# Performance work log

Measured on AMD Instinct MI355X. Metric: run time of the kernel, lower is better.

The kernel has to match this reference:

```python
import jax, jax.numpy as jnp
import numpy as np


def setup_inputs() -> dict:
    key = jax.random.key(0)
    k1, k2, k3 = jax.random.split(key, 3)
    N = 16384
    y = jax.random.normal(k1, (N,), dtype=jnp.float32)
    y_hat = jax.random.normal(k2, (N,), dtype=jnp.float32)
    status = jax.random.randint(k3, (N,), 0, 2, dtype=jnp.int32)
    return {"y": y, "y_hat": y_hat, "status": status}


def reference(y, y_hat, status):
    # Pairwise concordance index over all pairs i < j.
    # ge[i, j] = y[i] >= y[j]; le[i, j] = y[i] <= y[j]
    N = y.shape[0]
    ge = y[:, None] >= y[None, :]
    le = y[:, None] <= y[None, :]
    ge_hat = y_hat[:, None] >= y_hat[None, :]
    le_hat = y_hat[:, None] <= y_hat[None, :]
    st_i = (status == 1)[:, None]  # astatus_1 broadcast over j
    st_j = (status == 1)[None, :]  # bstatus_1 broadcast over i
    # upper-triangular mask (strict): pairs with j > i
    mask = jnp.triu(jnp.ones((N, N), dtype=bool), k=1)

    c1 = ge & ge_hat & st_j
    c2 = le & le_hat & st_i
    cc = (c1 | c2) & mask

    tp1 = le & st_i
    tp2 = ge & st_j
    tp = (tp1 | tp2) & mask

    c = jnp.sum(cc.astype(jnp.int32)).astype(jnp.float32)
    total_pairs = jnp.sum(tp.astype(jnp.int32)).astype(jnp.float32)
    return c / total_pairs
```

## Files before the change

kernel.cpp:

```cpp
#include <hip/hip_runtime.h>


#define BLOCK 256
#define TI 256
#define TJ 512
#define GRID_MAIN 1024


__global__ __launch_bounds__(256) void compact_kernel(
    const float* __restrict__ y, const float* __restrict__ yh,
    const int* __restrict__ status, int n,
    unsigned* __restrict__ cnts,
    float* __restrict__ y1, float* __restrict__ yh1,
    float* __restrict__ y0, float* __restrict__ yh0)
{
    int i = blockIdx.x * 256 + threadIdx.x;
    int lane = threadIdx.x & 63;
    bool act = i < n;
    float yv  = act ? y[i]  : 0.0f;
    float yhv = act ? yh[i] : 0.0f;
    bool st = act && (status[i] == 1);
    unsigned long long m1 = __ballot(st);
    unsigned long long m0 = __ballot(act && !st);
    unsigned long long lt = (lane == 63) ? ~0ull >> 1 : ((1ull << lane) - 1ull);
    unsigned b1 = 0, b0 = 0;
    if (lane == 0) {
        b1 = atomicAdd(&cnts[0], (unsigned)__popcll(m1));
        b0 = atomicAdd(&cnts[1], (unsigned)__popcll(m0));
    }
    b1 = __shfl(b1, 0, 64);
    b0 = __shfl(b0, 0, 64);
    if (st) {
        unsigned s = b1 + (unsigned)__popcll(m1 & lt);
        y1[s] = yv; yh1[s] = yhv;
    } else if (act) {
        unsigned s = b0 + (unsigned)__popcll(m0 & lt);
        y0[s] = yv; yh0[s] = yhv;
    }
}

__global__ __launch_bounds__(BLOCK) void pairs_kernel(
    const unsigned* __restrict__ cnts,
    const float* __restrict__ y1, const float* __restrict__ yh1,
    const float* __restrict__ y0, const float* __restrict__ yh0,
    unsigned long long* __restrict__ acc)
{
    __shared__ __align__(16) float2 s_yy[TJ];
    const int tid = threadIdx.x;
    const unsigned K = cnts[0], M = cnts[1];
    const int ntJ  = (int)((K + TJ - 1) / TJ);
    const int ntIA = (int)((K + TI - 1) / TI);
    const int ntIB = (int)((M + TI - 1) / TI);
    const int ntA  = ntIA * ntJ;
    const int ntot = ntA + ntIB * ntJ;

    const float PINF = __int_as_float(0x7f800000);
    const float NINF = __int_as_float(0xff800000);

    unsigned accA = 0, accBc = 0, accBt = 0;

    for (int t = blockIdx.x; t < ntot; t += gridDim.x) {
        bool isA = t < ntA;
        int tt = isA ? t : t - ntA;
        int ti = tt / ntJ;
        int tj = tt - ti * ntJ;
        int jbase = tj * TJ;
        int jcnt = (int)K - jbase; if (jcnt > TJ) jcnt = TJ;

        for (int s = tid; s < TJ; s += BLOCK) {
            bool inb = s < jcnt;
            int j = jbase + s;
            float a = inb ? y1[j]  : PINF;
            float b = inb ? yh1[j] : NINF;
            s_yy[s] = make_float2(a, b);
        }
        __syncthreads();

        int i = ti * TI + tid;
        unsigned ilim = isA ? K : M;
        const float* py = isA ? y1  : y0;
        const float* ph = isA ? yh1 : yh0;
        bool iv = (unsigned)i < ilim;
        float yi  = iv ? py[i] : NINF;
        float yhi = iv ? ph[i] : NINF;

        if (isA) {
            unsigned ax = 0;
#pragma unroll 8
            for (int jj = 0; jj < TJ; ++jj) {
                float2 p = s_yy[jj];
                ax += (unsigned)((yi >= p.x) != (yhi >= p.y));
            }
            if (iv) accA += (unsigned)TJ - ax;
        } else {
            unsigned bg = 0, bc = 0;
#pragma unroll 8
            for (int jj = 0; jj < TJ; ++jj) {
                float2 p = s_yy[jj];
                bool ge = yi >= p.x;
                bool gh = yhi >= p.y;
                bg += (unsigned)ge;
                bc += (unsigned)(ge & gh);
            }
            accBt += bg; accBc += bc;
        }
        __syncthreads();
    }

#pragma unroll
    for (int off = 32; off > 0; off >>= 1) {
        accA  += __shfl_down(accA,  off, 64);
        accBc += __shfl_down(accBc, off, 64);
        accBt += __shfl_down(accBt, off, 64);
    }
    __shared__ unsigned rA[4], rC[4], rT[4];
    int wav = tid >> 6, lane = tid & 63;
    if (lane == 0) { rA[wav] = accA; rC[wav] = accBc; rT[wav] = accBt; }
    __syncthreads();
    if (tid == 0) {
        unsigned long long a = rA[0] + rA[1] + rA[2] + rA[3];
        unsigned long long c = rC[0] + rC[1] + rC[2] + rC[3];
        unsigned long long t = rT[0] + rT[1] + rT[2] + rT[3];
        if (a) atomicAdd(&acc[0], a);
        if (c) atomicAdd(&acc[1], c);
        if (t) atomicAdd(&acc[2], t);
    }
}

__global__ void finalize_kernel(const unsigned* __restrict__ cnts,
                                const unsigned long long* __restrict__ acc,
                                float* __restrict__ out)
{
    if (threadIdx.x == 0) {
        unsigned long long K = cnts[0];
        unsigned long long CC = acc[0] + 2ull * acc[1];
        unsigned long long TP = K * K + 2ull * acc[2];
        long long cn = (long long)CC - (long long)K;
        long long tn = (long long)TP - (long long)K;
        out[0] = (float)cn / (float)tn;
    }
}

extern "C" void kernel_launch(void* const* d_in, const int* in_sizes, int n_in,
                              void* d_out, int out_size, void* d_ws, size_t ws_size,
                              hipStream_t stream) {
    const float* y      = (const float*)d_in[0];
    const float* y_hat  = (const float*)d_in[1];
    const int*   status = (const int*)d_in[2];
    float* out = (float*)d_out;
    int n = in_sizes[0];

    char* base = (char*)d_ws;
    unsigned* cnts = (unsigned*)base;
    unsigned long long* acc = (unsigned long long*)(base + 8);
    float* y1  = (float*)(base + 64);
    float* yh1 = y1 + n;
    float* y0  = yh1 + n;
    float* yh0 = y0 + n;

    hipMemsetAsync(base, 0, 32, stream);

    hipLaunchKernelGGL(compact_kernel, dim3((n + 255) / 256), dim3(256), 0, stream,
                       y, y_hat, status, n, cnts, y1, yh1, y0, yh0);

    hipLaunchKernelGGL(pairs_kernel, dim3(GRID_MAIN), dim3(BLOCK), 0, stream,
                       cnts, y1, yh1, y0, yh0, acc);

    hipLaunchKernelGGL(finalize_kernel, dim3(1), dim3(64), 0, stream,
                       cnts, acc, out);
}
```

Measured before the change: 94.94 us.

## Register-block four i-values per thread and pad compacted arrays with sentinels

Each thread now holds four i elements in registers, so every shared-memory j load is reused four times and the LDS read traffic per comparison falls. The y and y_hat arrays are interleaved into float2 and padded to multiples of 1024 with infinity sentinels written by a new fill kernel. This removes the bounds checks in the tile loads, and the padding contribution is subtracted analytically in finalize. The cost is a larger i-tile, which can waste work on padding and lowers the number of tiles, plus an extra kernel that fills the workspace.

```diff
diff --git a/kernel.cpp b/kernel.cpp
--- a/kernel.cpp
+++ b/kernel.cpp
@@ -2,17 +2,29 @@
 
 
 #define BLOCK 256
-#define TI 256
-#define TJ 512
-#define GRID_MAIN 1024
+#define TJ 256
+#define IT 4
+#define TI (BLOCK * IT)
+#define GRID_PAIRS 1024
 
+
+__global__ __launch_bounds__(256) void fill_kernel(
+    float2* __restrict__ p1, float2* __restrict__ p0, int stride,
+    unsigned* __restrict__ hdr)
+{
+    int i = blockIdx.x * 256 + threadIdx.x;
+    if (i < stride) {
+        p1[i] = make_float2(__int_as_float(0x7f800000), __int_as_float(0xff800000));
+        p0[i] = make_float2(__int_as_float(0xff800000), __int_as_float(0xff800000));
+    }
+    if (blockIdx.x == 0 && threadIdx.x < 8) hdr[threadIdx.x] = 0u;
+}
 
 __global__ __launch_bounds__(256) void compact_kernel(
     const float* __restrict__ y, const float* __restrict__ yh,
     const int* __restrict__ status, int n,
     unsigned* __restrict__ cnts,
-    float* __restrict__ y1, float* __restrict__ yh1,
-    float* __restrict__ y0, float* __restrict__ yh0)
+    float2* __restrict__ p1, float2* __restrict__ p0)
 {
     int i = blockIdx.x * 256 + threadIdx.x;
     int lane = threadIdx.x & 63;
@@ -22,7 +34,7 @@
     bool st = act && (status[i] == 1);
     unsigned long long m1 = __ballot(st);
     unsigned long long m0 = __ballot(act && !st);
-    unsigned long long lt = (lane == 63) ? ~0ull >> 1 : ((1ull << lane) - 1ull);
+    unsigned long long lt = (1ull << lane) - 1ull;
     unsigned b1 = 0, b0 = 0;
     if (lane == 0) {
         b1 = atomicAdd(&cnts[0], (unsigned)__popcll(m1));
@@ -31,99 +43,93 @@
     b1 = __shfl(b1, 0, 64);
     b0 = __shfl(b0, 0, 64);
     if (st) {
-        unsigned s = b1 + (unsigned)__popcll(m1 & lt);
-        y1[s] = yv; yh1[s] = yhv;
+        p1[b1 + (unsigned)__popcll(m1 & lt)] = make_float2(yv, yhv);
     } else if (act) {
-        unsigned s = b0 + (unsigned)__popcll(m0 & lt);
-        y0[s] = yv; yh0[s] = yhv;
+        p0[b0 + (unsigned)__popcll(m0 & lt)] = make_float2(yv, yhv);
     }
 }
 
 __global__ __launch_bounds__(BLOCK) void pairs_kernel(
     const unsigned* __restrict__ cnts,
-    const float* __restrict__ y1, const float* __restrict__ yh1,
-    const float* __restrict__ y0, const float* __restrict__ yh0,
+    const float2* __restrict__ p1, const float2* __restrict__ p0,
     unsigned long long* __restrict__ acc)
 {
-    __shared__ __align__(16) float2 s_yy[TJ];
+    __shared__ float2 s_j[TJ];
     const int tid = threadIdx.x;
     const unsigned K = cnts[0], M = cnts[1];
-    const int ntJ  = (int)((K + TJ - 1) / TJ);
-    const int ntIA = (int)((K + TI - 1) / TI);
-    const int ntIB = (int)((M + TI - 1) / TI);
+    const int Kp = (int)((K + 1023u) & ~1023u);
+    const int Mp = (int)((M + 1023u) & ~1023u);
+    const int ntJ  = Kp >> 8;
+    const int ntIA = Kp >> 10;
+    const int ntIB = Mp >> 10;
     const int ntA  = ntIA * ntJ;
     const int ntot = ntA + ntIB * ntJ;
 
-    const float PINF = __int_as_float(0x7f800000);
-    const float NINF = __int_as_float(0xff800000);
-
-    unsigned accA = 0, accBc = 0, accBt = 0;
+    unsigned accNE = 0, accBC = 0, accBG = 0;
 
     for (int t = blockIdx.x; t < ntot; t += gridDim.x) {
         bool isA = t < ntA;
         int tt = isA ? t : t - ntA;
         int ti = tt / ntJ;
         int tj = tt - ti * ntJ;
-        int jbase = tj * TJ;
-        int jcnt = (int)K - jbase; if (jcnt > TJ) jcnt = TJ;
 
-        for (int s = tid; s < TJ; s += BLOCK) {
-            bool inb = s < jcnt;
-            int j = jbase + s;
-            float a = inb ? y1[j]  : PINF;
-            float b = inb ? yh1[j] : NINF;
-            s_yy[s] = make_float2(a, b);
-        }
+        s_j[tid] = p1[tj * TJ + tid];
         __syncthreads();
 
-        int i = ti * TI + tid;
-        unsigned ilim = isA ? K : M;
-        const float* py = isA ? y1  : y0;
-        const float* ph = isA ? yh1 : yh0;
-        bool iv = (unsigned)i < ilim;
-        float yi  = iv ? py[i] : NINF;
-        float yhi = iv ? ph[i] : NINF;
+        const float2* pi = isA ? p1 : p0;
+        int ib = ti * TI + tid;
+        float2 v0 = pi[ib];
+        float2 v1 = pi[ib + BLOCK];
+        float2 v2 = pi[ib + 2 * BLOCK];
+        float2 v3 = pi[ib + 3 * BLOCK];
 
         if (isA) {
-            unsigned ax = 0;
+            unsigned n0 = 0, n1 = 0;
 #pragma unroll 8
             for (int jj = 0; jj < TJ; ++jj) {
-                float2 p = s_yy[jj];
-                ax += (unsigned)((yi >= p.x) != (yhi >= p.y));
+                float2 p = s_j[jj];
+                n0 += (unsigned)((v0.x >= p.x) != (v0.y >= p.y));
+                n1 += (unsigned)((v1.x >= p.x) != (v1.y >= p.y));
+                n0 += (unsigned)((v2.x >= p.x) != (v2.y >= p.y));
+                n1 += (unsigned)((v3.x >= p.x) != (v3.y >= p.y));
             }
-            if (iv) accA += (unsigned)TJ - ax;
+            accNE += n0 + n1;
         } else {
-            unsigned bg = 0, bc = 0;
+            unsigned g0 = 0, g1 = 0, c0 = 0, c1 = 0;
 #pragma unroll 8
             for (int jj = 0; jj < TJ; ++jj) {
-                float2 p = s_yy[jj];
-                bool ge = yi >= p.x;
-                bool gh = yhi >= p.y;
-                bg += (unsigned)ge;
-                bc += (unsigned)(ge & gh);
+                float2 p = s_j[jj];
+                bool a0 = v0.x >= p.x, b0 = v0.y >= p.y;
+                bool a1 = v1.x >= p.x, b1 = v1.y >= p.y;
+                bool a2 = v2.x >= p.x, b2 = v2.y >= p.y;
+                bool a3 = v3.x >= p.x, b3 = v3.y >= p.y;
+                g0 += (unsigned)a0; c0 += (unsigned)(a0 & b0);
+                g1 += (unsigned)a1; c1 += (unsigned)(a1 & b1);
+                g0 += (unsigned)a2; c0 += (unsigned)(a2 & b2);
+                g1 += (unsigned)a3; c1 += (unsigned)(a3 & b3);
             }
-            accBt += bg; accBc += bc;
+            accBG += g0 + g1; accBC += c0 + c1;
         }
         __syncthreads();
     }
 
 #pragma unroll
     for (int off = 32; off > 0; off >>= 1) {
-        accA  += __shfl_down(accA,  off, 64);
-        accBc += __shfl_down(accBc, off, 64);
-        accBt += __shfl_down(accBt, off, 64);
+        accNE += __shfl_down(accNE, off, 64);
+        accBC += __shfl_down(accBC, off, 64);
+        accBG += __shfl_down(accBG, off, 64);
     }
-    __shared__ unsigned rA[4], rC[4], rT[4];
+    __shared__ unsigned rN[4], rC[4], rG[4];
     int wav = tid >> 6, lane = tid & 63;
-    if (lane == 0) { rA[wav] = accA; rC[wav] = accBc; rT[wav] = accBt; }
+    if (lane == 0) { rN[wav] = accNE; rC[wav] = accBC; rG[wav] = accBG; }
     __syncthreads();
     if (tid == 0) {
-        unsigned long long a = rA[0] + rA[1] + rA[2] + rA[3];
-        unsigned long long c = rC[0] + rC[1] + rC[2] + rC[3];
-        unsigned long long t = rT[0] + rT[1] + rT[2] + rT[3];
-        if (a) atomicAdd(&acc[0], a);
-        if (c) atomicAdd(&acc[1], c);
-        if (t) atomicAdd(&acc[2], t);
+        unsigned long long ne = (unsigned long long)rN[0] + rN[1] + rN[2] + rN[3];
+        unsigned long long bc = (unsigned long long)rC[0] + rC[1] + rC[2] + rC[3];
+        unsigned long long bg = (unsigned long long)rG[0] + rG[1] + rG[2] + rG[3];
+        if (ne) atomicAdd(&acc[0], ne);
+        if (bc) atomicAdd(&acc[1], bc);
+        if (bg) atomicAdd(&acc[2], bg);
     }
 }
 
@@ -133,7 +139,9 @@
 {
     if (threadIdx.x == 0) {
         unsigned long long K = cnts[0];
-        unsigned long long CC = acc[0] + 2ull * acc[1];
+        unsigned long long Kp = (K + 1023ull) & ~1023ull;
+        unsigned long long pad = Kp - K;
+        unsigned long long CC = Kp * Kp - acc[0] - pad * pad + 2ull * acc[1];
         unsigned long long TP = K * K + 2ull * acc[2];
         long long cn = (long long)CC - (long long)K;
         long long tn = (long long)TP - (long long)K;
@@ -149,22 +157,22 @@
     const int*   status = (const int*)d_in[2];
     float* out = (float*)d_out;
     int n = in_sizes[0];
+    int stride = n + 1024;
 
     char* base = (char*)d_ws;
     unsigned* cnts = (unsigned*)base;
     unsigned long long* acc = (unsigned long long*)(base + 8);
-    float* y1  = (float*)(base + 64);
-    float* yh1 = y1 + n;
-    float* y0  = yh1 + n;
-    float* yh0 = y0 + n;
+    float2* p1 = (float2*)(base + 64);
+    float2* p0 = p1 + stride;
 
-    hipMemsetAsync(base, 0, 32, stream);
+    hipLaunchKernelGGL(fill_kernel, dim3((stride + 255) / 256), dim3(256), 0, stream,
+                       p1, p0, stride, cnts);
 
     hipLaunchKernelGGL(compact_kernel, dim3((n + 255) / 256), dim3(256), 0, stream,
-                       y, y_hat, status, n, cnts, y1, yh1, y0, yh0);
+                       y, y_hat, status, n, cnts, p1, p0);
 
-    hipLaunchKernelGGL(pairs_kernel, dim3(GRID_MAIN), dim3(BLOCK), 0, stream,
-                       cnts, y1, yh1, y0, yh0, acc);
+    hipLaunchKernelGGL(pairs_kernel, dim3(GRID_PAIRS), dim3(BLOCK), 0, stream,
+                       cnts, p1, p0, acc);
 
     hipLaunchKernelGGL(finalize_kernel, dim3(1), dim3(64), 0, stream,
                        cnts, acc, out);
```

Result: no change. 95.31 us (+0.4%).
